# Performance work log

Hardware: AMD Instinct MI355X
Metric: run time of the kernel (lower is better)

Reference implementation:

```python
import jax, jax.numpy as jnp
import numpy as np

B, T, C = 4, 2048, 1024
NUM_EXPERTS = 8
TOP_K = 2
D_EXPERT = 4 * C * TOP_K // NUM_EXPERTS  # 1024


def setup_inputs() -> dict:
    key = jax.random.key(0)
    k0, k1, k2, k3 = jax.random.split(key, 4)
    x = jax.random.normal(k0, (B, T, C), dtype=jnp.float32)
    # nn.Linear(n_embd, num_experts, bias=False).weight has shape [E, C]
    router_w = jax.random.normal(k1, (NUM_EXPERTS, C), dtype=jnp.float32) * 0.02
    # w1_all = stack of c_fc.weight.T  -> [E, C, D]
    w1_all = jax.random.normal(k2, (NUM_EXPERTS, C, D_EXPERT), dtype=jnp.float32) * 0.02
    # w2_all = stack of c_proj.weight.T -> [E, D, C]
    w2_all = jax.random.normal(k3, (NUM_EXPERTS, D_EXPERT, C), dtype=jnp.float32) * 0.02
    return {"x": x, "router_w": router_w, "w1_all": w1_all, "w2_all": w2_all}


def reference(x, router_w, w1_all, w2_all):
    b, t, c = x.shape
    x_flat = x.reshape(-1, c)                      # [N, C]
    router_logits = x_flat @ router_w.T            # [N, E]
    top_k_logits, top_k_idx = jax.lax.top_k(router_logits, TOP_K)  # [N, K]
    router_probs = jax.nn.softmax(top_k_logits, axis=-1)           # [N, K]

    # Same math as the original per-token weight gather, but computed as
    # dense all-expert GEMMs followed by an output gather (avoids the
    # [N, K, C, D] materialized weight copies while producing identical values).
    hidden = jnp.einsum('nc,ecd->ned', x_flat, w1_all)   # [N, E, D]
    hidden = jnp.square(jax.nn.relu(hidden))             # relu^2
    out_all = jnp.einsum('ned,edc->nec', hidden, w2_all) # [N, E, C]

    sel = jnp.take_along_axis(out_all, top_k_idx[:, :, None], axis=1)  # [N, K, C]
    out = jnp.sum(sel * router_probs[:, :, None], axis=1)             # [N, C]
    return out.reshape(b, t, c)
```

## Files before the change

### kernel.cpp

```cpp
#include <hip/hip_runtime.h>
#include <cstdint>
#include <cstddef>

typedef unsigned short ushort_t;
typedef unsigned short ushort8 __attribute__((ext_vector_type(8)));
typedef __bf16 bf16x8 __attribute__((ext_vector_type(8)));
typedef float floatx4 __attribute__((ext_vector_type(4)));

#define N_TOK 8192
#define CDIM 1024
#define NEXP 8

__device__ __forceinline__ float bf2f(ushort_t h) {
  union { unsigned int u; float f; } v; v.u = ((unsigned int)h) << 16; return v.f;
}
__device__ __forceinline__ ushort_t f2bf(float f) {
  union { float f; unsigned int u; } v; v.f = f;
  unsigned int r = v.u + 0x7fffu + ((v.u >> 16) & 1u);
  return (ushort_t)(r >> 16);
}

__device__ __forceinline__ void async_copy16(const ushort_t* g, ushort_t* l) {
  __builtin_amdgcn_global_load_lds(
      (const __attribute__((address_space(1))) unsigned int*)g,
      (__attribute__((address_space(3))) unsigned int*)l, 16, 0, 0);
}

__device__ __forceinline__ int detect_f32(const ushort_t* x) {
  ushort_t u = x[threadIdx.x & 127];
  int ex = (u >> 7) & 0xFF;
  int crazy = (ex >= 0xC0 || ex <= 0x30) ? 1 : 0;
  int total = __syncthreads_count(crazy);
  return (total >= 32) ? 1 : 0;
}

__global__ void fused_front(const void* __restrict__ xv,
                            const void* __restrict__ rwv,
                            const void* __restrict__ w1v,
                            const void* __restrict__ w2v,
                            int* __restrict__ cnt,
                            int* __restrict__ tok_e,
                            float* __restrict__ prob,
                            ushort_t* __restrict__ xbf,
                            ushort_t* __restrict__ w1T,
                            ushort_t* __restrict__ w2T) {
  int isf32 = detect_f32((const ushort_t*)xv);
  int bid = blockIdx.x;

  if (bid < 2048) {
    if (bid == 0 && threadIdx.x < NEXP) cnt[threadIdx.x] = 0;
    int wid = threadIdx.x >> 6;
    int lane = threadIdx.x & 63;
    int t = bid * 4 + wid;

    float acc[NEXP];
#pragma unroll
    for (int e = 0; e < NEXP; e++) acc[e] = 0.f;

    if (isf32) {
      const float* xr = (const float*)xv + (size_t)t * CDIM;
      const float* rw = (const float*)rwv;
#pragma unroll
      for (int half = 0; half < 2; half++) {
        int base = (lane + half * 64) * 8;
        floatx4 x0 = *(const floatx4*)(xr + base);
        floatx4 x1 = *(const floatx4*)(xr + base + 4);
        ushort8 o;
#pragma unroll
        for (int i = 0; i < 4; i++) { o[i] = f2bf(x0[i]); o[4 + i] = f2bf(x1[i]); }
        *(ushort8*)(xbf + (size_t)t * CDIM + base) = o;
#pragma unroll
        for (int e = 0; e < NEXP; e++) {
          floatx4 w0 = *(const floatx4*)(rw + e * CDIM + base);
          floatx4 w1 = *(const floatx4*)(rw + e * CDIM + base + 4);
          acc[e] += x0[0]*w0[0] + x0[1]*w0[1] + x0[2]*w0[2] + x0[3]*w0[3]
                  + x1[0]*w1[0] + x1[1]*w1[1] + x1[2]*w1[2] + x1[3]*w1[3];
        }
      }
    } else {
      const ushort_t* xr = (const ushort_t*)xv + (size_t)t * CDIM;
      const ushort_t* rw = (const ushort_t*)rwv;
#pragma unroll
      for (int half = 0; half < 2; half++) {
        int base = (lane + half * 64) * 8;
        ushort8 xu = *(const ushort8*)(xr + base);
        *(ushort8*)(xbf + (size_t)t * CDIM + base) = xu;
#pragma unroll
        for (int e = 0; e < NEXP; e++) {
          ushort8 wu = *(const ushort8*)(rw + e * CDIM + base);
#pragma unroll
          for (int i = 0; i < 8; i++) acc[e] += bf2f(xu[i]) * bf2f(wu[i]);
        }
      }
    }

#pragma unroll
    for (int e = 0; e < NEXP; e++) {
#pragma unroll
      for (int off = 32; off > 0; off >>= 1) acc[e] += __shfl_xor(acc[e], off);
    }

    if (lane == 0) {
      int e0 = 0; float l0 = acc[0];
#pragma unroll
      for (int e = 1; e < NEXP; e++) if (acc[e] > l0) { l0 = acc[e]; e0 = e; }
      int e1 = (e0 == 0) ? 1 : 0; float l1 = acc[e1];
#pragma unroll
      for (int e = 0; e < NEXP; e++) {
        if (e != e0 && acc[e] > l1) { l1 = acc[e]; e1 = e; }
      }
      float p0 = 1.f / (1.f + __expf(l1 - l0));
      tok_e[t] = e0 | (e1 << 8);
      prob[t * 2] = p0;
      prob[t * 2 + 1] = 1.f - p0;
    }
  } else {
    int b2 = bid - 2048;
    int z = b2 >> 8;
    int by = (b2 >> 4) & 15;
    int bx = b2 & 15;
    size_t moff = (size_t)(z & 7) << 20;
    const void* srcv = (z < 8) ? w1v : w2v;
    ushort_t* dst = ((z < 8) ? w1T : w2T) + moff;

    __shared__ __align__(16) ushort_t tile[64][72];
    int t = threadIdx.x;
    int R0 = by * 64, C0 = bx * 64;
    int r = t >> 2, cb = (t & 3) * 16;
    if (isf32) {
      const float* sp = (const float*)srcv + moff + (size_t)(R0 + r) * 1024 + C0 + cb;
      ushort8 o0, o1;
#pragma unroll
      for (int q = 0; q < 2; q++) {
        floatx4 f = *(const floatx4*)(sp + q * 4);
#pragma unroll
        for (int i = 0; i < 4; i++) o0[q * 4 + i] = f2bf(f[i]);
      }
#pragma unroll
      for (int q = 0; q < 2; q++) {
        floatx4 f = *(const floatx4*)(sp + 8 + q * 4);
#pragma unroll
        for (int i = 0; i < 4; i++) o1[q * 4 + i] = f2bf(f[i]);
      }
      *(ushort8*)&tile[r][cb] = o0;
      *(ushort8*)&tile[r][cb + 8] = o1;
    } else {
      const ushort_t* sp = (const ushort_t*)srcv + moff + (size_t)(R0 + r) * 1024 + C0 + cb;
      *(ushort8*)&tile[r][cb] = *(const ushort8*)sp;
      *(ushort8*)&tile[r][cb + 8] = *(const ushort8*)(sp + 8);
    }
    __syncthreads();
    int d = t >> 2, rb = (t & 3) * 16;
    ushort8 o0, o1;
#pragma unroll
    for (int j = 0; j < 8; j++) { o0[j] = tile[rb + j][d]; o1[j] = tile[rb + 8 + j][d]; }
    ushort_t* dp = dst + (size_t)(C0 + d) * 1024 + R0 + rb;
    *(ushort8*)dp = o0;
    *(ushort8*)(dp + 8) = o1;
  }
}

__global__ void scatter_kernel(const int* __restrict__ tok_e,
                               int* __restrict__ cnt,
                               int* __restrict__ slots) {
  __shared__ int lcnt[NEXP];
  __shared__ int gbase[NEXP];
  int tid = threadIdx.x;
  if (tid < NEXP) lcnt[tid] = 0;
  __syncthreads();
  int t = blockIdx.x * 1024 + tid;
  int ee = tok_e[t];
  int e0 = ee & 0xFF, e1 = (ee >> 8) & 0xFF;
  int lofs0 = atomicAdd(&lcnt[e0], 1);
  int lofs1 = atomicAdd(&lcnt[e1], 1);
  __syncthreads();
  if (tid < NEXP) gbase[tid] = atomicAdd(&cnt[tid], lcnt[tid]);
  __syncthreads();
  slots[e0 * N_TOK + gbase[e0] + lofs0] = t * 2;
  slots[e1 * N_TOK + gbase[e1] + lofs1] = t * 2 + 1;
}

template <int MODE>
__global__ __launch_bounds__(512, 4) void moe_gemm(const ushort_t* __restrict__ A,
                                                   const ushort_t* __restrict__ BT,
                                                   ushort_t* __restrict__ Out,
                                                   const int* __restrict__ cnt,
                                                   const int* __restrict__ slots,
                                                   const float* __restrict__ prob) {
  int bid = blockIdx.x;
  int e = bid & 7;
  int nt = (bid >> 3) & 7;
  int mt = bid >> 6;
  int M = cnt[e];
  M = (M > N_TOK) ? N_TOK : M;
  int m0 = mt * 256;
  if (m0 >= M) return;
  int n0 = nt * 128;

  __shared__ __align__(16) ushort_t As[256 * 64];
  __shared__ __align__(16) ushort_t Bs[128 * 64];
  __shared__ int srow[256];

  int tid = threadIdx.x;
  if (tid < 256) {
    int gm = m0 + tid;
    int gi = (gm < M) ? gm : (M - 1);
    srow[tid] = slots[e * N_TOK + gi] & (2 * N_TOK - 1);
  }
  __syncthreads();

  int wid = tid >> 6;
  int lane = tid & 63;
  int lrow = lane >> 3;
  int gchunk = (lane & 7) ^ lrow;

  const ushort_t* aptr[4];
  const ushort_t* bptr[2];
  int arowbase = wid * 32;
  int browbase = wid * 16;
#pragma unroll
  for (int j = 0; j < 4; j++) {
    int rr = arowbase + j * 8 + lrow;
    int s = srow[rr];
    int aidx = (MODE == 0) ? (s >> 1) : s;
    aptr[j] = A + (size_t)aidx * CDIM + gchunk * 8;
  }
#pragma unroll
  for (int j = 0; j < 2; j++) {
    int rr = browbase + j * 8 + lrow;
    bptr[j] = BT + ((size_t)e << 20) + (size_t)(n0 + rr) * 1024 + gchunk * 8;
  }
  ushort_t* albase = &As[arowbase * 64];
  ushort_t* blbase = &Bs[browbase * 64];

  int wm = (wid >> 1) * 64;
  int wn = (wid & 1) * 64;
  int qd = lane >> 4;
  int ln = lane & 15;
  int l7 = ln & 7;

  floatx4 zero = {0.f, 0.f, 0.f, 0.f};
  floatx4 acc[4][4];
#pragma unroll
  for (int i = 0; i < 4; i++)
#pragma unroll
    for (int j = 0; j < 4; j++) acc[i][j] = zero;

  for (int k0 = 0; k0 < 1024; k0 += 64) {
    __syncthreads();
#pragma unroll
    for (int j = 0; j < 4; j++) async_copy16(aptr[j] + k0, albase + j * 512);
#pragma unroll
    for (int j = 0; j < 2; j++) async_copy16(bptr[j] + k0, blbase + j * 512);
    __syncthreads();
#pragma unroll
    for (int ks = 0; ks < 2; ks++) {
      bf16x8 afr[4], bfr[4];
#pragma unroll
      for (int i = 0; i < 4; i++) {
        int pc = ((ks * 4 + qd) ^ l7) * 8;
        afr[i] = *(const bf16x8*)&As[(wm + i * 16 + ln) * 64 + pc];
        bfr[i] = *(const bf16x8*)&Bs[(wn + i * 16 + ln) * 64 + pc];
      }
#pragma unroll
      for (int i = 0; i < 4; i++)
#pragma unroll
        for (int j = 0; j < 4; j++)
          acc[i][j] = __builtin_amdgcn_mfma_f32_16x16x32_bf16(afr[i], bfr[j], acc[i][j], 0, 0, 0);
    }
  }

#pragma unroll
  for (int i = 0; i < 4; i++) {
#pragma unroll
    for (int r = 0; r < 4; r++) {
      int rl = wm + i * 16 + qd * 4 + r;
      int gm = m0 + rl;
      if (gm >= M) continue;
      int s = srow[rl];
      float p = (MODE == 1) ? prob[s] : 0.f;
      ushort_t* orow = Out + (size_t)s * 1024 + n0 + wn + ln;
#pragma unroll
      for (int j = 0; j < 4; j++) {
        float v = acc[i][j][r];
        if (MODE == 0) { v = fmaxf(v, 0.f); v = v * v; }
        else v *= p;
        orow[j * 16] = f2bf(v);
      }
    }
  }
}

__global__ void combine_kernel(const ushort_t* __restrict__ oslots,
                               float* __restrict__ out) {
  int idx = (blockIdx.x * 256 + threadIdx.x) * 8;
  int t = idx >> 10;
  int c = idx & 1023;
  const ushort_t* r0 = oslots + ((size_t)t * 2) * 1024 + c;
  const ushort_t* r1 = r0 + 1024;
  ushort8 a = *(const ushort8*)r0;
  ushort8 b = *(const ushort8*)r1;
  floatx4 o0, o1;
#pragma unroll
  for (int i = 0; i < 4; i++) o0[i] = bf2f(a[i]) + bf2f(b[i]);
#pragma unroll
  for (int i = 0; i < 4; i++) o1[i] = bf2f(a[4 + i]) + bf2f(b[4 + i]);
  *(floatx4*)(out + idx) = o0;
  *(floatx4*)(out + idx + 4) = o1;
}

extern "C" void kernel_launch(void* const* d_in, const int* in_sizes, int n_in,
                              void* d_out, int out_size, void* d_ws, size_t ws_size,
                              hipStream_t stream) {
  const void* x  = d_in[0];
  const void* rw = d_in[1];
  const void* w1 = d_in[2];
  const void* w2 = d_in[3];
  float* out = (float*)d_out;
  char* ws = (char*)d_ws;

  int* cnt  = (int*)(ws + 0);
  int* slots = (int*)(ws + 1024);
  float* prob = (float*)(ws + 263168);
  int* tok_e = (int*)(ws + 335872);
  ushort_t* xbf = (ushort_t*)(ws + 524288);
  ushort_t* w1T = (ushort_t*)(ws + 17301504);
  ushort_t* hidden = (ushort_t*)(ws + 34078720);
  ushort_t* w2T = (ushort_t*)(ws + 67633152);
  ushort_t* oslots = (ushort_t*)(ws + 524288);

  fused_front<<<6144, 256, 0, stream>>>(x, rw, w1, w2, cnt, tok_e, prob,
                                        xbf, w1T, w2T);
  scatter_kernel<<<NEXP, 1024, 0, stream>>>(tok_e, cnt, slots);
  moe_gemm<0><<<2048, 512, 0, stream>>>(xbf, w1T, hidden, cnt, slots, prob);
  moe_gemm<1><<<2048, 512, 0, stream>>>(hidden, w2T, oslots, cnt, slots, prob);
  combine_kernel<<<4096, 256, 0, stream>>>(oslots, out);
}
```

Baseline: 263.9 us.

## Fuse top-k combine into second GEMM epilogue via fp32 atomic adds

Drops the separate combine kernel and the bf16 per-slot output buffer. The second expert GEMM now scales each result by its router probability and atomically adds it into the fp32 output, which extra blocks in the front kernel zero first. This removes one launch and a round trip of 32 MB through memory, but adds global fp32 atomics with scattered row addresses, and the summation order of the two experts is no longer fixed.

Measured after the change: 302.0 us. +14.5%, slower.

```diff
diff --git a/kernel.cpp b/kernel.cpp
--- a/kernel.cpp
+++ b/kernel.cpp
@@ -43,9 +43,19 @@
                             float* __restrict__ prob,
                             ushort_t* __restrict__ xbf,
                             ushort_t* __restrict__ w1T,
-                            ushort_t* __restrict__ w2T) {
+                            ushort_t* __restrict__ w2T,
+                            float* __restrict__ out) {
+  int bid = blockIdx.x;
+
+  if (bid >= 6144) {
+    float* p = out + ((size_t)(bid - 6144) * 256 + threadIdx.x) * 16;
+    floatx4 z = {0.f, 0.f, 0.f, 0.f};
+#pragma unroll
+    for (int q = 0; q < 4; q++) *(floatx4*)(p + q * 4) = z;
+    return;
+  }
+
   int isf32 = detect_f32((const ushort_t*)xv);
-  int bid = blockIdx.x;
 
   if (bid < 2048) {
     if (bid == 0 && threadIdx.x < NEXP) cnt[threadIdx.x] = 0;
@@ -184,6 +194,7 @@
 __global__ __launch_bounds__(512, 4) void moe_gemm(const ushort_t* __restrict__ A,
                                                    const ushort_t* __restrict__ BT,
                                                    ushort_t* __restrict__ Out,
+                                                   float* __restrict__ OutF,
                                                    const int* __restrict__ cnt,
                                                    const int* __restrict__ slots,
                                                    const float* __restrict__ prob) {
@@ -278,35 +289,24 @@
       int gm = m0 + rl;
       if (gm >= M) continue;
       int s = srow[rl];
-      float p = (MODE == 1) ? prob[s] : 0.f;
-      ushort_t* orow = Out + (size_t)s * 1024 + n0 + wn + ln;
-#pragma unroll
-      for (int j = 0; j < 4; j++) {
-        float v = acc[i][j][r];
-        if (MODE == 0) { v = fmaxf(v, 0.f); v = v * v; }
-        else v *= p;
-        orow[j * 16] = f2bf(v);
-      }
-    }
-  }
-}
-
-__global__ void combine_kernel(const ushort_t* __restrict__ oslots,
-                               float* __restrict__ out) {
-  int idx = (blockIdx.x * 256 + threadIdx.x) * 8;
-  int t = idx >> 10;
-  int c = idx & 1023;
-  const ushort_t* r0 = oslots + ((size_t)t * 2) * 1024 + c;
-  const ushort_t* r1 = r0 + 1024;
-  ushort8 a = *(const ushort8*)r0;
-  ushort8 b = *(const ushort8*)r1;
-  floatx4 o0, o1;
-#pragma unroll
-  for (int i = 0; i < 4; i++) o0[i] = bf2f(a[i]) + bf2f(b[i]);
-#pragma unroll
-  for (int i = 0; i < 4; i++) o1[i] = bf2f(a[4 + i]) + bf2f(b[4 + i]);
-  *(floatx4*)(out + idx) = o0;
-  *(floatx4*)(out + idx + 4) = o1;
+      if (MODE == 0) {
+        ushort_t* orow = Out + (size_t)s * 1024 + n0 + wn + ln;
+#pragma unroll
+        for (int j = 0; j < 4; j++) {
+          float v = acc[i][j][r];
+          v = fmaxf(v, 0.f); v = v * v;
+          orow[j * 16] = f2bf(v);
+        }
+      } else {
+        float p = prob[s];
+        float* orow = OutF + (size_t)(s >> 1) * 1024 + n0 + wn + ln;
+#pragma unroll
+        for (int j = 0; j < 4; j++) {
+          atomicAdd(&orow[j * 16], acc[i][j][r] * p);
+        }
+      }
+    }
+  }
 }
 
 extern "C" void kernel_launch(void* const* d_in, const int* in_sizes, int n_in,
@@ -327,12 +327,10 @@
   ushort_t* w1T = (ushort_t*)(ws + 17301504);
   ushort_t* hidden = (ushort_t*)(ws + 34078720);
   ushort_t* w2T = (ushort_t*)(ws + 67633152);
-  ushort_t* oslots = (ushort_t*)(ws + 524288);
-
-  fused_front<<<6144, 256, 0, stream>>>(x, rw, w1, w2, cnt, tok_e, prob,
-                                        xbf, w1T, w2T);
+
+  fused_front<<<8192, 256, 0, stream>>>(x, rw, w1, w2, cnt, tok_e, prob,
+                                        xbf, w1T, w2T, out);
   scatter_kernel<<<NEXP, 1024, 0, stream>>>(tok_e, cnt, slots);
-  moe_gemm<0><<<2048, 512, 0, stream>>>(xbf, w1T, hidden, cnt, slots, prob);
-  moe_gemm<1><<<2048, 512, 0, stream>>>(hidden, w2T, oslots, cnt, slots, prob);
-  combine_kernel<<<4096, 256, 0, stream>>>(oslots, out);
-}
+  moe_gemm<0><<<2048, 512, 0, stream>>>(xbf, w1T, hidden, nullptr, cnt, slots, prob);
+  moe_gemm<1><<<2048, 512, 0, stream>>>(hidden, w2T, nullptr, out, cnt, slots, prob);
+}
```

## Triple-buffer LDS tiles with async prefetch and barrier-split MFMA phases

Applied to the files above, without the earlier changes.

Replaces the single-buffered K loop, which had a sync-load-sync-compute pattern, with a three-stage LDS ring. Global-to-LDS copies are issued two tiles ahead, and vmcnt waits let loads overlap MFMA work. Each k-step is split into barrier-separated phases with s_setprio around the MFMA bursts to interleave LDS reads and math across waves. The shared-memory footprint triples to about 144KB, and launch bounds drop from 4 to 2 blocks per SM, which reduces occupancy.

New measurement: 302.4 us. 1.15x slower.

```diff
diff --git a/kernel.cpp b/kernel.cpp
--- a/kernel.cpp
+++ b/kernel.cpp
@@ -181,7 +181,7 @@
 }
 
 template <int MODE>
-__global__ __launch_bounds__(512, 4) void moe_gemm(const ushort_t* __restrict__ A,
+__global__ __launch_bounds__(512, 2) void moe_gemm(const ushort_t* __restrict__ A,
                                                    const ushort_t* __restrict__ BT,
                                                    ushort_t* __restrict__ Out,
                                                    const int* __restrict__ cnt,
@@ -197,8 +197,8 @@
   if (m0 >= M) return;
   int n0 = nt * 128;
 
-  __shared__ __align__(16) ushort_t As[256 * 64];
-  __shared__ __align__(16) ushort_t Bs[128 * 64];
+  __shared__ __align__(16) ushort_t As[3][256 * 64];
+  __shared__ __align__(16) ushort_t Bs[3][128 * 64];
   __shared__ int srow[256];
 
   int tid = threadIdx.x;
@@ -230,8 +230,6 @@
     int rr = browbase + j * 8 + lrow;
     bptr[j] = BT + ((size_t)e << 20) + (size_t)(n0 + rr) * 1024 + gchunk * 8;
   }
-  ushort_t* albase = &As[arowbase * 64];
-  ushort_t* blbase = &Bs[browbase * 64];
 
   int wm = (wid >> 1) * 64;
   int wn = (wid & 1) * 64;
@@ -246,29 +244,80 @@
 #pragma unroll
     for (int j = 0; j < 4; j++) acc[i][j] = zero;
 
-  for (int k0 = 0; k0 < 1024; k0 += 64) {
-    __syncthreads();
-#pragma unroll
-    for (int j = 0; j < 4; j++) async_copy16(aptr[j] + k0, albase + j * 512);
-#pragma unroll
-    for (int j = 0; j < 2; j++) async_copy16(bptr[j] + k0, blbase + j * 512);
-    __syncthreads();
-#pragma unroll
-    for (int ks = 0; ks < 2; ks++) {
-      bf16x8 afr[4], bfr[4];
-#pragma unroll
-      for (int i = 0; i < 4; i++) {
-        int pc = ((ks * 4 + qd) ^ l7) * 8;
-        afr[i] = *(const bf16x8*)&As[(wm + i * 16 + ln) * 64 + pc];
-        bfr[i] = *(const bf16x8*)&Bs[(wn + i * 16 + ln) * 64 + pc];
-      }
-#pragma unroll
-      for (int i = 0; i < 4; i++)
-#pragma unroll
-        for (int j = 0; j < 4; j++)
-          acc[i][j] = __builtin_amdgcn_mfma_f32_16x16x32_bf16(afr[i], bfr[j], acc[i][j], 0, 0, 0);
-    }
-  }
+#define STAGE(b, kt)                                                          \
+  do {                                                                        \
+    _Pragma("unroll")                                                         \
+    for (int j = 0; j < 4; j++)                                               \
+      async_copy16(aptr[j] + (kt) * 64, &As[b][arowbase * 64] + j * 512);     \
+    _Pragma("unroll")                                                         \
+    for (int j = 0; j < 2; j++)                                               \
+      async_copy16(bptr[j] + (kt) * 64, &Bs[b][browbase * 64] + j * 512);     \
+  } while (0)
+
+#define PHASE_PAIR(cb, ks)                                                    \
+  do {                                                                        \
+    int pc = (((ks) * 4 + qd) ^ l7) * 8;                                      \
+    bf16x8 a0 = *(const bf16x8*)&As[cb][(wm + 0 * 16 + ln) * 64 + pc];        \
+    bf16x8 a1 = *(const bf16x8*)&As[cb][(wm + 1 * 16 + ln) * 64 + pc];        \
+    bf16x8 b0 = *(const bf16x8*)&Bs[cb][(wn + 0 * 16 + ln) * 64 + pc];        \
+    bf16x8 b1 = *(const bf16x8*)&Bs[cb][(wn + 1 * 16 + ln) * 64 + pc];        \
+    bf16x8 b2 = *(const bf16x8*)&Bs[cb][(wn + 2 * 16 + ln) * 64 + pc];        \
+    bf16x8 b3 = *(const bf16x8*)&Bs[cb][(wn + 3 * 16 + ln) * 64 + pc];        \
+    __builtin_amdgcn_s_barrier();                                             \
+    asm volatile("s_waitcnt lgkmcnt(0)" ::: "memory");                        \
+    __builtin_amdgcn_s_setprio(1);                                            \
+    acc[0][0] = __builtin_amdgcn_mfma_f32_16x16x32_bf16(a0, b0, acc[0][0], 0, 0, 0); \
+    acc[0][1] = __builtin_amdgcn_mfma_f32_16x16x32_bf16(a0, b1, acc[0][1], 0, 0, 0); \
+    acc[0][2] = __builtin_amdgcn_mfma_f32_16x16x32_bf16(a0, b2, acc[0][2], 0, 0, 0); \
+    acc[0][3] = __builtin_amdgcn_mfma_f32_16x16x32_bf16(a0, b3, acc[0][3], 0, 0, 0); \
+    acc[1][0] = __builtin_amdgcn_mfma_f32_16x16x32_bf16(a1, b0, acc[1][0], 0, 0, 0); \
+    acc[1][1] = __builtin_amdgcn_mfma_f32_16x16x32_bf16(a1, b1, acc[1][1], 0, 0, 0); \
+    acc[1][2] = __builtin_amdgcn_mfma_f32_16x16x32_bf16(a1, b2, acc[1][2], 0, 0, 0); \
+    acc[1][3] = __builtin_amdgcn_mfma_f32_16x16x32_bf16(a1, b3, acc[1][3], 0, 0, 0); \
+    __builtin_amdgcn_s_setprio(0);                                            \
+    __builtin_amdgcn_s_barrier();                                             \
+    bf16x8 a2 = *(const bf16x8*)&As[cb][(wm + 2 * 16 + ln) * 64 + pc];        \
+    bf16x8 a3 = *(const bf16x8*)&As[cb][(wm + 3 * 16 + ln) * 64 + pc];        \
+    __builtin_amdgcn_s_barrier();                                             \
+    asm volatile("s_waitcnt lgkmcnt(0)" ::: "memory");                        \
+    __builtin_amdgcn_s_setprio(1);                                            \
+    acc[2][0] = __builtin_amdgcn_mfma_f32_16x16x32_bf16(a2, b0, acc[2][0], 0, 0, 0); \
+    acc[2][1] = __builtin_amdgcn_mfma_f32_16x16x32_bf16(a2, b1, acc[2][1], 0, 0, 0); \
+    acc[2][2] = __builtin_amdgcn_mfma_f32_16x16x32_bf16(a2, b2, acc[2][2], 0, 0, 0); \
+    acc[2][3] = __builtin_amdgcn_mfma_f32_16x16x32_bf16(a2, b3, acc[2][3], 0, 0, 0); \
+    acc[3][0] = __builtin_amdgcn_mfma_f32_16x16x32_bf16(a3, b0, acc[3][0], 0, 0, 0); \
+    acc[3][1] = __builtin_amdgcn_mfma_f32_16x16x32_bf16(a3, b1, acc[3][1], 0, 0, 0); \
+    acc[3][2] = __builtin_amdgcn_mfma_f32_16x16x32_bf16(a3, b2, acc[3][2], 0, 0, 0); \
+    acc[3][3] = __builtin_amdgcn_mfma_f32_16x16x32_bf16(a3, b3, acc[3][3], 0, 0, 0); \
+    __builtin_amdgcn_s_setprio(0);                                            \
+    __builtin_amdgcn_s_barrier();                                             \
+  } while (0)
+
+#define TILE(cb, sb, kt, WN)                                                  \
+  do {                                                                        \
+    if ((kt) + 2 < 16) STAGE(sb, (kt) + 2);                                   \
+    asm volatile("s_waitcnt vmcnt(" #WN ")" ::: "memory");                    \
+    __builtin_amdgcn_s_barrier();                                             \
+    PHASE_PAIR(cb, 0);                                                        \
+    PHASE_PAIR(cb, 1);                                                        \
+  } while (0)
+
+  STAGE(0, 0);
+  STAGE(1, 1);
+  for (int it = 0; it < 4; ++it) {
+    int kt = it * 3;
+    TILE(0, 2, kt, 12);
+    TILE(1, 0, kt + 1, 12);
+    TILE(2, 1, kt + 2, 12);
+  }
+  TILE(0, 2, 12, 12);
+  TILE(1, 0, 13, 12);
+  TILE(2, 1, 14, 6);
+  TILE(0, 1, 15, 0);
+
+#undef STAGE
+#undef PHASE_PAIR
+#undef TILE
 
 #pragma unroll
   for (int i = 0; i < 4; i++) {
```
